# Kernel tuning notes

Measured on AMD Instinct MI355X. Metric: run time of the kernel, lower is better.

Reference implementation:

```python
import jax, jax.numpy as jnp
import numpy as np

B, N, DIM = 4, 2048, 1024
HEADS, DH = 16, 64
INNER = HEADS * DH
SCALE = 8.0
EPS = 1e-5


def setup_inputs() -> dict:
    key = jax.random.key(0)
    ks = jax.random.split(key, 8)
    x = jax.random.normal(ks[0], (B, N, DIM), dtype=jnp.float32)
    context_mask = jax.random.bernoulli(ks[1], 0.9, (B, N))
    gamma = jnp.ones((DIM,), dtype=jnp.float32)
    null_kv = jax.random.normal(ks[2], (2, HEADS, 1, DH), dtype=jnp.float32)
    Wq = jax.random.normal(ks[3], (DIM, INNER), dtype=jnp.float32) * 0.02
    Wkv = jax.random.normal(ks[4], (DIM, 2 * INNER), dtype=jnp.float32) * 0.02
    # q_scale init: scale / dim_head**-0.5 = 8 * sqrt(64) = 64
    q_scale = jnp.full((DH,), SCALE * (DH ** 0.5), dtype=jnp.float32)
    k_scale = jnp.ones((DH,), dtype=jnp.float32)
    Wout = jax.random.normal(ks[5], (INNER, DIM), dtype=jnp.float32) * 0.02
    return {"x": x, "context_mask": context_mask, "gamma": gamma,
            "null_kv": null_kv, "Wq": Wq, "Wkv": Wkv,
            "q_scale": q_scale, "k_scale": k_scale, "Wout": Wout}


def _l2norm(t):
    return t / jnp.sqrt(jnp.sum(t * t, axis=-1, keepdims=True) + 1e-12)


def reference(x, context_mask, gamma, null_kv, Wq, Wkv, q_scale, k_scale, Wout):
    b, n, _ = x.shape
    # LayerNorm (beta buffer is zeros)
    mu = jnp.mean(x, axis=-1, keepdims=True)
    var = jnp.mean((x - mu) ** 2, axis=-1, keepdims=True)
    xn = (x - mu) / jnp.sqrt(var + EPS) * gamma
    # projections
    q = (xn @ Wq).reshape(b, n, HEADS, DH)
    kv = xn @ Wkv
    k = kv[..., :INNER].reshape(b, n, HEADS, DH)
    v = kv[..., INNER:].reshape(b, n, HEADS, DH)
    # null kv token: [h,1,d] -> [b,1,h,d]
    nk = jnp.broadcast_to(null_kv[0].transpose(1, 0, 2)[None], (b, 1, HEADS, DH))
    nv = jnp.broadcast_to(null_kv[1].transpose(1, 0, 2)[None], (b, 1, HEADS, DH))
    k = jnp.concatenate([nk, k], axis=1)  # [b, n+1, h, d]
    v = jnp.concatenate([nv, v], axis=1)
    # cosine-sim attention with learned per-dim scales
    q = _l2norm(q) * q_scale
    k = _l2norm(k) * k_scale
    # bias from mask (padded True for null token)
    mask = jnp.pad(context_mask, ((0, 0), (1, 0)), constant_values=True)
    bias = jnp.where(mask, 0.0, -10000.0)[:, None, None, :]  # [b,1,1,n+1]
    # memory_efficient_attention applies 1/sqrt(dh) internally
    scores = jnp.einsum('bqhd,bkhd->bhqk', q, k) * (DH ** -0.5) + bias
    attn = jax.nn.softmax(scores, axis=-1)
    out = jnp.einsum('bhqk,bkhd->bqhd', attn, v).reshape(b, n, INNER)
    return out @ Wout
```

## Files before the change

kernel.cpp:

```cpp
#include <hip/hip_runtime.h>
#include <hip/hip_bf16.h>
#include <stdint.h>


using f32x4  = __attribute__((ext_vector_type(4))) float;
using bf16x8 = __attribute__((ext_vector_type(8))) __bf16;
using f16x8  = __attribute__((ext_vector_type(8))) _Float16;
using uintv4 = __attribute__((ext_vector_type(4))) unsigned int;

__device__ __forceinline__ float b2f(unsigned short u) {
    return __uint_as_float(((unsigned)u) << 16);
}
__device__ __forceinline__ unsigned short f2b(float f) {
    unsigned u = __float_as_uint(f);
    u += 0x7fffu + ((u >> 16) & 1u);
    return (unsigned short)(u >> 16);
}
__device__ __forceinline__ unsigned short f2h(float f) {
    return __builtin_bit_cast(unsigned short, (_Float16)f);
}
__device__ __forceinline__ f32x4 mfma16(bf16x8 a, bf16x8 b, f32x4 c) {
    return __builtin_amdgcn_mfma_f32_16x16x32_bf16(a, b, c, 0, 0, 0);
}
__device__ __forceinline__ f32x4 mfma16h(f16x8 a, f16x8 b, f32x4 c) {
    return __builtin_amdgcn_mfma_f32_16x16x32_f16(a, b, c, 0, 0, 0);
}
__device__ __forceinline__ unsigned pk16(float a, float b) {
    return __builtin_bit_cast(unsigned, __builtin_amdgcn_cvt_pkrtz(a, b));
}
__device__ __forceinline__ void gl_lds16(const void* g, void* l) {
    __builtin_amdgcn_global_load_lds(
        (const __attribute__((address_space(1))) unsigned int*)g,
        (__attribute__((address_space(3))) unsigned int*)l, 16, 0, 0);
}

__global__ __launch_bounds__(256) void transpose_f2b(
    const float* __restrict__ in, unsigned short* __restrict__ out,
    int R, int C)
{
    __shared__ unsigned short t[32][33];
    int tx = threadIdx.x, ty = threadIdx.y;
    int c = blockIdx.x * 32 + tx;
#pragma unroll
    for (int i = 0; i < 4; ++i) {
        int r = blockIdx.y * 32 + ty + i * 8;
        t[ty + i * 8][tx] = f2b(in[(size_t)r * C + c]);
    }
    __syncthreads();
    int r2 = blockIdx.y * 32 + tx;
#pragma unroll
    for (int i = 0; i < 4; ++i) {
        int c2 = blockIdx.x * 32 + ty + i * 8;
        out[(size_t)c2 * R + r2] = t[tx][ty + i * 8];
    }
}

__global__ __launch_bounds__(256) void ln_kernel(
    const float* __restrict__ x, const float* __restrict__ gamma,
    unsigned short* __restrict__ xn)
{
    int row = blockIdx.x, tid = threadIdx.x;
    int wave = tid >> 6, lane = tid & 63;
    float4 raw = *(const float4*)(x + ((size_t)row << 10) + (tid << 2));
    float v[4] = { raw.x, raw.y, raw.z, raw.w };
    float s  = v[0] + v[1] + v[2] + v[3];
    float s2 = v[0]*v[0] + v[1]*v[1] + v[2]*v[2] + v[3]*v[3];
#pragma unroll
    for (int off = 1; off < 64; off <<= 1) {
        s  += __shfl_xor(s, off);
        s2 += __shfl_xor(s2, off);
    }
    __shared__ float ps[4], ps2[4], sh[2];
    if (lane == 0) { ps[wave] = s; ps2[wave] = s2; }
    __syncthreads();
    if (tid == 0) {
        float S  = ps[0] + ps[1] + ps[2] + ps[3];
        float S2 = ps2[0] + ps2[1] + ps2[2] + ps2[3];
        float mu  = S * (1.f / 1024.f);
        float var = S2 * (1.f / 1024.f) - mu * mu;
        sh[0] = mu; sh[1] = rsqrtf(var + 1e-5f);
    }
    __syncthreads();
    float mu = sh[0], rstd = sh[1];
    float4 g4 = *(const float4*)(gamma + (tid << 2));
    float g[4] = { g4.x, g4.y, g4.z, g4.w };
    unsigned short o[4];
#pragma unroll
    for (int i = 0; i < 4; ++i) o[i] = f2b((v[i] - mu) * rstd * g[i]);
    uint2 out;
    out.x = (unsigned)o[0] | ((unsigned)o[1] << 16);
    out.y = (unsigned)o[2] | ((unsigned)o[3] << 16);
    *(uint2*)(xn + ((size_t)row << 10) + (tid << 2)) = out;
}

template<int MODE>
__global__ __launch_bounds__(256, 2) void gemm_bt(
    const unsigned short* __restrict__ A, const unsigned short* __restrict__ Bt,
    void* __restrict__ Cout, const float* __restrict__ scale,
    unsigned short* __restrict__ Vout,
    int M, int N, int K, int ldc)
{
    __shared__ __bf16 As[128 * 32];
    __shared__ __bf16 Bs[128 * 32];
    int tid = threadIdx.x, lane = tid & 63, wave = tid >> 6;
    int quad = lane >> 4, l15 = lane & 15;
    int m0 = blockIdx.y * 128, n0 = blockIdx.x * 128;
    int wm = (wave & 1) * 64, wn = (wave >> 1) * 64;
    f32x4 acc[4][4] = {};

    const int srow = wave * 32 + (lane >> 2);
    const int scol = (lane & 3) << 3;
    const unsigned short* gA = A  + (size_t)(m0 + srow) * K + scol;
    const unsigned short* gB = Bt + (size_t)(n0 + srow) * K + scol;
    __bf16* lA0 = &As[(wave * 32) * 32];
    __bf16* lA1 = &As[(wave * 32 + 16) * 32];
    __bf16* lB0 = &Bs[(wave * 32) * 32];
    __bf16* lB1 = &Bs[(wave * 32 + 16) * 32];
    const size_t rstep = (size_t)16 * K;

    for (int k0 = 0; k0 < K; k0 += 32) {
        gl_lds16(gA,         lA0);
        gl_lds16(gA + rstep, lA1);
        gl_lds16(gB,         lB0);
        gl_lds16(gB + rstep, lB1);
        gA += 32; gB += 32;
        __syncthreads();
        bf16x8 af[4], bfv[4];
#pragma unroll
        for (int i = 0; i < 4; ++i)
            af[i] = *(const bf16x8*)&As[(wm + i * 16 + l15) * 32 + quad * 8];
#pragma unroll
        for (int j = 0; j < 4; ++j)
            bfv[j] = *(const bf16x8*)&Bs[(wn + j * 16 + l15) * 32 + quad * 8];
#pragma unroll
        for (int i = 0; i < 4; ++i)
#pragma unroll
            for (int j = 0; j < 4; ++j)
                acc[i][j] = mfma16(af[i], bfv[j], acc[i][j]);
        __syncthreads();
    }

    if (MODE == 2) {
#pragma unroll
        for (int i = 0; i < 4; ++i)
#pragma unroll
            for (int j = 0; j < 4; ++j) {
                int row = m0 + wm + i * 16 + quad * 4;
                int col = n0 + wn + j * 16 + l15;
                size_t base = (size_t)row * ldc + col;
#pragma unroll
                for (int r = 0; r < 4; ++r)
                    ((float*)Cout)[base + (size_t)r * ldc] = acc[i][j][r];
            }
        return;
    }

    if constexpr (MODE == 1) {
        const bool isv = (n0 + wn) >= 1024;
        if (isv) {
            __shared__ unsigned short Vx[4][64 * 64];
            unsigned short* tileL = Vx[wave];
            int hv = (n0 + wn - 1024) >> 6;
            int bidx = m0 >> 11;
            int tok0w = (m0 + wm) & 2047;
            size_t vbase = (size_t)((((bidx << 4) + hv) << 6)) * 2056;
#pragma unroll
            for (int i = 0; i < 4; ++i)
#pragma unroll
                for (int j = 0; j < 4; ++j) {
                    int d = j * 16 + l15;
                    int tk = (i * 16 + quad * 4) ^ ((d & 7) << 3);
                    unsigned u01 = (unsigned)f2h(acc[i][j][0])
                                 | ((unsigned)f2h(acc[i][j][1]) << 16);
                    unsigned u23 = (unsigned)f2h(acc[i][j][2])
                                 | ((unsigned)f2h(acc[i][j][3]) << 16);
                    *(unsigned*)&tileL[d * 64 + tk]     = u01;
                    *(unsigned*)&tileL[d * 64 + tk + 2] = u23;
                }
#pragma unroll
            for (int rr = 0; rr < 16; ++rr) {
                int d = rr * 4 + quad;
                uint2 val = *(const uint2*)
                    &tileL[d * 64 + ((l15 * 4) ^ ((d & 7) << 3))];
                *(uint2*)(Vout + vbase + (size_t)d * 2056 + tok0w + l15 * 4) = val;
            }
            return;
        }
    }

    float sc[4];
#pragma unroll
    for (int j = 0; j < 4; ++j) {
        float s = scale[j * 16 + l15];
        sc[j] = (MODE == 0) ? s * (0.125f * 1.44269504088896f) : s;
    }
#pragma unroll
    for (int i = 0; i < 4; ++i)
#pragma unroll
        for (int r = 0; r < 4; ++r) {
            float ss = 0.f;
#pragma unroll
            for (int j = 0; j < 4; ++j) ss += acc[i][j][r] * acc[i][j][r];
            ss += __shfl_xor(ss, 1); ss += __shfl_xor(ss, 2);
            ss += __shfl_xor(ss, 4); ss += __shfl_xor(ss, 8);
            float mul = rsqrtf(ss + 1e-12f);
            size_t rowbase = (size_t)(m0 + wm + i * 16 + quad * 4 + r) * ldc
                           + n0 + wn + l15;
#pragma unroll
            for (int j = 0; j < 4; ++j) {
                float v = acc[i][j][r];
                ((unsigned short*)Cout)[rowbase + j * 16] = f2b(v * mul * sc[j]);
            }
        }
}

__global__ __launch_bounds__(256) void nullkv_kernel(
    const float* __restrict__ null_kv, const float* __restrict__ k_scale,
    unsigned short* __restrict__ knull, unsigned short* __restrict__ Vt)
{
    int wave = threadIdx.x >> 6, lane = threadIdx.x & 63;
    int h = blockIdx.x * 4 + wave;
    int idx = (h << 6) + lane;
    float kvl = null_kv[idx];
    float ss = kvl * kvl;
#pragma unroll
    for (int off = 1; off < 64; off <<= 1) ss += __shfl_xor(ss, off);
    knull[idx] = f2b(kvl * rsqrtf(ss + 1e-12f) * k_scale[lane]);
    unsigned short vn = f2h(null_kv[1024 + idx]);
#pragma unroll
    for (int b = 0; b < 4; ++b)
        Vt[((size_t)(((b << 4) + h) << 6) + lane) * 2056 + 2048] = vn;
    int t = blockIdx.x * 256 + threadIdx.x;
#pragma unroll
    for (int rr = 0; rr < 4; ++rr) {
        size_t row = (size_t)t * 4 + rr;
#pragma unroll
        for (int c = 0; c < 7; ++c)
            Vt[row * 2056 + 2049 + c] = 0;
    }
}

__global__ __launch_bounds__(256, 3) void attn_kernel(
    const unsigned short* __restrict__ qn,
    const unsigned short* __restrict__ kvK,
    const unsigned short* __restrict__ knull,
    const unsigned short* __restrict__ Vt,
    const int* __restrict__ mask,
    unsigned short* __restrict__ ao)
{
    __shared__ __bf16    Kt[2][64 * 64];
    __shared__ _Float16  Vl[2][64 * 64];
    __shared__ __align__(16) float biasLds[2][64];

    const int tid = threadIdx.x, lane = tid & 63, wave = tid >> 6;
    const int quad = lane >> 4, l15 = lane & 15;
    const int bh = blockIdx.x;
    const int b = bh >> 4, h = bh & 15;
    const int mbase = blockIdx.y * 128 + wave * 32;
    const size_t rowoff = (size_t)b * 2048;

    bf16x8 qf[2][2];
#pragma unroll
    for (int rg = 0; rg < 2; ++rg)
#pragma unroll
        for (int ks = 0; ks < 2; ++ks)
            qf[rg][ks] = *(const bf16x8*)
                &qn[((rowoff + mbase + rg * 16 + l15) << 10) + (h << 6) + ks * 32 + quad * 8];

    const int t8  = lane >> 3;
    const int w7  = lane & 7;
    const int ksc = (w7 ^ t8) << 3;
    const size_t vrow0 = ((size_t)bh << 6);

    const int r0v = wave * 16 + t8;
    const int r1v = wave * 16 + 8 + t8;
    auto Tof = [](int r) {
        return ((r >> 5) << 5) | (((r >> 2) & 3) << 3)
             | (((r >> 4) & 1) << 2) | (r & 3);
    };
    const int T0 = Tof(r0v), T1 = Tof(r1v);

    const unsigned short* kp0 = kvK + ((rowoff + T0) << 10) + (h << 6) + ksc;
    const unsigned short* kp1 = kvK + ((rowoff + T1) << 10) + (h << 6) + ksc;
    const unsigned short* vp0 = Vt + (vrow0 + r0v) * 2056 + ((w7 ^ t8) << 3);
    const unsigned short* vp1 = Vt + (vrow0 + r1v) * 2056 + ((w7 ^ t8) << 3);

    auto issueFast = [&](int bf) {
        gl_lds16(kp0, &Kt[bf][(wave * 16) * 64]);
        gl_lds16(kp1, &Kt[bf][(wave * 16 + 8) * 64]);
        gl_lds16(vp0, &Vl[bf][(wave * 16) * 64]);
        gl_lds16(vp1, &Vl[bf][(wave * 16 + 8) * 64]);
        kp0 += 65536; kp1 += 65536;
        vp0 += 64; vp1 += 64;
    };
    auto issue32 = [&](int bf) {
        const unsigned short* kc =
            kvK + ((rowoff + 2047) << 10) + (h << 6) + ksc;
        const unsigned short* s0 = (T0 == 0) ? knull + (h << 6) + ksc : kc;
        gl_lds16(s0, &Kt[bf][(wave * 16) * 64]);
        gl_lds16(kc, &Kt[bf][(wave * 16 + 8) * 64]);
        gl_lds16(Vt + (vrow0 + r0v) * 2056 + 2048, &Vl[bf][(wave * 16) * 64]);
        gl_lds16(Vt + (vrow0 + r1v) * 2056 + 2048, &Vl[bf][(wave * 16 + 8) * 64]);
    };
    auto biasFor = [&](int nt) -> float {
        int j = (nt << 6) + lane;
        float bv = -512.f;
        if (j < 2048) { if (mask[(b << 11) + j] != 0) bv = 0.f; }
        else if (j == 2048) bv = 0.f;
        return bv;
    };

    const uintv4 onesu = { 0x3c003c00u, 0x3c003c00u, 0x3c003c00u, 0x3c003c00u };
    const f16x8 ones = __builtin_bit_cast(f16x8, onesu);

    f32x4 O[2][4] = {};
    f32x4 rsacc[2] = {};

    issueFast(0);
    float bcur = 0.f;
    if (wave == 0) bcur = biasFor(0);

    for (int nt = 0; nt < 33; ++nt) {
        const int buf = nt & 1;
        if (wave == 0) biasLds[buf][lane] = bcur;
        __syncthreads();
        if (nt < 31) {
            issueFast(buf ^ 1);
            if (wave == 0) bcur = biasFor(nt + 1);
        } else if (nt == 31) {
            issue32(buf ^ 1);
            if (wave == 0) bcur = biasFor(32);
        }

#pragma unroll
        for (int g = 0; g < 2; ++g) {
            float4 b0 = *(const float4*)&biasLds[buf][(g << 5) + (quad << 3)];
            float4 b1 = *(const float4*)&biasLds[buf][(g << 5) + (quad << 3) + 4];
            f32x4 s[2][2];
#pragma unroll
            for (int rg = 0; rg < 2; ++rg) {
                s[rg][0] = f32x4{ b0.x, b0.y, b0.z, b0.w };
                s[rg][1] = f32x4{ b1.x, b1.y, b1.z, b1.w };
            }
#pragma unroll
            for (int t = 0; t < 2; ++t) {
                const __bf16* kb = &Kt[buf][((g * 2 + t) * 16 + l15) * 64];
                bf16x8 k0 = *(const bf16x8*)&kb[(quad ^ (l15 & 7)) << 3];
                bf16x8 k1 = *(const bf16x8*)&kb[((4 + quad) ^ (l15 & 7)) << 3];
#pragma unroll
                for (int rg = 0; rg < 2; ++rg) {
                    s[rg][t] = mfma16(k0, qf[rg][0], s[rg][t]);
                    s[rg][t] = mfma16(k1, qf[rg][1], s[rg][t]);
                }
            }
            f16x8 vf8[4];
#pragma unroll
            for (int dt = 0; dt < 4; ++dt)
                vf8[dt] = *(const f16x8*)
                    &Vl[buf][(dt * 16 + l15) * 64
                             + ((((g << 2) + quad) ^ (l15 & 7)) << 3)];
#pragma unroll
            for (int rg = 0; rg < 2; ++rg) {
                float e0 = __builtin_amdgcn_exp2f(s[rg][0][0]);
                float e1 = __builtin_amdgcn_exp2f(s[rg][0][1]);
                float e2 = __builtin_amdgcn_exp2f(s[rg][0][2]);
                float e3 = __builtin_amdgcn_exp2f(s[rg][0][3]);
                float e4 = __builtin_amdgcn_exp2f(s[rg][1][0]);
                float e5 = __builtin_amdgcn_exp2f(s[rg][1][1]);
                float e6 = __builtin_amdgcn_exp2f(s[rg][1][2]);
                float e7 = __builtin_amdgcn_exp2f(s[rg][1][3]);
                uintv4 pu = { pk16(e0, e1), pk16(e2, e3),
                              pk16(e4, e5), pk16(e6, e7) };
                f16x8 p = __builtin_bit_cast(f16x8, pu);
                rsacc[rg] = mfma16h(p, ones, rsacc[rg]);
#pragma unroll
                for (int dt = 0; dt < 4; ++dt)
                    O[rg][dt] = mfma16h(p, vf8[dt], O[rg][dt]);
            }
        }
    }

#pragma unroll
    for (int rg = 0; rg < 2; ++rg) {
        float inv[4];
#pragma unroll
        for (int r = 0; r < 4; ++r) inv[r] = 1.f / rsacc[rg][r];
#pragma unroll
        for (int dt = 0; dt < 4; ++dt) {
            size_t base = ((rowoff + mbase + rg * 16 + quad * 4) << 10)
                        + (h << 6) + dt * 16 + l15;
#pragma unroll
            for (int r = 0; r < 4; ++r)
                ao[base + ((size_t)r << 10)] = f2b(O[rg][dt][r] * inv[r]);
        }
    }
}

extern "C" void kernel_launch(void* const* d_in, const int* in_sizes, int n_in,
                              void* d_out, int out_size, void* d_ws, size_t ws_size,
                              hipStream_t stream)
{
    const float* x       = (const float*)d_in[0];
    const int*   mask    = (const int*)d_in[1];
    const float* gamma   = (const float*)d_in[2];
    const float* null_kv = (const float*)d_in[3];
    const float* Wq      = (const float*)d_in[4];
    const float* Wkv     = (const float*)d_in[5];
    const float* q_scale = (const float*)d_in[6];
    const float* k_scale = (const float*)d_in[7];
    const float* Wout    = (const float*)d_in[8];

    char* ws = (char*)d_ws;
    const size_t VTG_OFF  = (size_t)48u << 20;
    const size_t VTG_SIZE = (size_t)4096 * 4112;
    unsigned short* xn    = (unsigned short*)(ws);
    unsigned short* ao    = xn;
    unsigned short* q     = (unsigned short*)(ws + ((size_t)16u << 20));
    unsigned short* kvK   = (unsigned short*)(ws + ((size_t)32u << 20));
    unsigned short* VtG   = (unsigned short*)(ws + VTG_OFF);
    unsigned short* WqT   = (unsigned short*)(ws + VTG_OFF + VTG_SIZE - ((size_t)2u << 20));
    unsigned short* WkvT  = (unsigned short*)(ws + VTG_OFF + VTG_SIZE);
    unsigned short* WoutT = (unsigned short*)(ws + VTG_OFF + VTG_SIZE + ((size_t)4u << 20));
    unsigned short* knull = (unsigned short*)(ws + VTG_OFF + VTG_SIZE + ((size_t)6u << 20));

    dim3 tb(32, 8);
    transpose_f2b<<<dim3(32, 32), tb, 0, stream>>>(Wq,   WqT,   1024, 1024);
    transpose_f2b<<<dim3(64, 32), tb, 0, stream>>>(Wkv,  WkvT,  1024, 2048);
    transpose_f2b<<<dim3(32, 32), tb, 0, stream>>>(Wout, WoutT, 1024, 1024);

    ln_kernel<<<8192, 256, 0, stream>>>(x, gamma, xn);

    gemm_bt<0><<<dim3(8, 64),  256, 0, stream>>>(xn, WqT, q, q_scale, nullptr,
                                                 8192, 1024, 1024, 1024);
    nullkv_kernel<<<4, 256, 0, stream>>>(null_kv, k_scale, knull, VtG);

    gemm_bt<1><<<dim3(16, 64), 256, 0, stream>>>(xn, WkvT, kvK, k_scale, VtG,
                                                 8192, 2048, 1024, 1024);

    attn_kernel<<<dim3(64, 16), 256, 0, stream>>>(q, kvK, knull, VtG, mask, ao);

    gemm_bt<2><<<dim3(8, 64), 256, 0, stream>>>(ao, WoutT, d_out, nullptr, nullptr,
                                                8192, 1024, 1024, 1024);
}
```

Before: 299.8 us.

## Double-buffer LDS tiles in bf16 GEMM to overlap global loads with MFMA

Doubles the shared-memory A and B tiles so the GEMM can stage K-slice s+1 into the alternate buffer while MFMAs run on slice s. One barrier per iteration is dropped, and the direct global-to-LDS loads for the next step are issued before the compute of the current one. This targets the exposed global-load latency in the projection and output GEMMs. In exchange, LDS use per block doubles to 32KB, which could limit occupancy, and correctness depends on the remaining end-of-loop barrier draining the async loads.

```diff
diff --git a/kernel.cpp b/kernel.cpp
--- a/kernel.cpp
+++ b/kernel.cpp
@@ -100,8 +100,8 @@
     unsigned short* __restrict__ Vout,
     int M, int N, int K, int ldc)
 {
-    __shared__ __bf16 As[128 * 32];
-    __shared__ __bf16 Bs[128 * 32];
+    __shared__ __bf16 As[2][128 * 32];
+    __shared__ __bf16 Bs[2][128 * 32];
     int tid = threadIdx.x, lane = tid & 63, wave = tid >> 6;
     int quad = lane >> 4, l15 = lane & 15;
     int m0 = blockIdx.y * 128, n0 = blockIdx.x * 128;
@@ -112,26 +112,31 @@
     const int scol = (lane & 3) << 3;
     const unsigned short* gA = A  + (size_t)(m0 + srow) * K + scol;
     const unsigned short* gB = Bt + (size_t)(n0 + srow) * K + scol;
-    __bf16* lA0 = &As[(wave * 32) * 32];
-    __bf16* lA1 = &As[(wave * 32 + 16) * 32];
-    __bf16* lB0 = &Bs[(wave * 32) * 32];
-    __bf16* lB1 = &Bs[(wave * 32 + 16) * 32];
     const size_t rstep = (size_t)16 * K;
-
-    for (int k0 = 0; k0 < K; k0 += 32) {
-        gl_lds16(gA,         lA0);
-        gl_lds16(gA + rstep, lA1);
-        gl_lds16(gB,         lB0);
-        gl_lds16(gB + rstep, lB1);
+    const int lo0 = (wave * 32) * 32;
+    const int lo1 = (wave * 32 + 16) * 32;
+
+    auto stage = [&](int bf) {
+        gl_lds16(gA,         &As[bf][lo0]);
+        gl_lds16(gA + rstep, &As[bf][lo1]);
+        gl_lds16(gB,         &Bs[bf][lo0]);
+        gl_lds16(gB + rstep, &Bs[bf][lo1]);
         gA += 32; gB += 32;
-        __syncthreads();
+    };
+
+    stage(0);
+    __syncthreads();
+    const int nsteps = K >> 5;
+    for (int s = 0; s < nsteps; ++s) {
+        const int cur = s & 1;
+        if (s + 1 < nsteps) stage(cur ^ 1);
         bf16x8 af[4], bfv[4];
 #pragma unroll
         for (int i = 0; i < 4; ++i)
-            af[i] = *(const bf16x8*)&As[(wm + i * 16 + l15) * 32 + quad * 8];
+            af[i] = *(const bf16x8*)&As[cur][(wm + i * 16 + l15) * 32 + quad * 8];
 #pragma unroll
         for (int j = 0; j < 4; ++j)
-            bfv[j] = *(const bf16x8*)&Bs[(wn + j * 16 + l15) * 32 + quad * 8];
+            bfv[j] = *(const bf16x8*)&Bs[cur][(wn + j * 16 + l15) * 32 + quad * 8];
 #pragma unroll
         for (int i = 0; i < 4; ++i)
 #pragma unroll
```

Result: no change. 305.2 us (+1.8%).
